# Kernel tuning notes

Measured on AMD Instinct MI355X. Metric: run time of the kernel, lower is better.

The kernel has to match this reference:

```python
import jax, jax.numpy as jnp
import numpy as np

B, N, D, H, ND = 16, 512, 768, 12, 32
DK = D // H  # 64
GRID = 11    # hard-coded 11x11 patch grid in SpatialCirclePosition.patch


def setup_inputs() -> dict:
    key = jax.random.key(0)
    ks = jax.random.split(key, 10)
    features = jax.random.normal(ks[0], (B, N, D), dtype=jnp.float32)
    boxes = jax.random.uniform(ks[1], (B, N, 4), dtype=jnp.float32)  # normalized [0,1]
    sizes_wh = jax.random.randint(ks[2], (B, 2), 512, 1024).astype(jnp.int32)
    image_sizes = jnp.concatenate([sizes_wh, sizes_wh], axis=-1)  # (B,4) = [w,h,w,h]
    s = 0.02
    Wq = jax.random.normal(ks[3], (D, D), dtype=jnp.float32) * s
    Wk = jax.random.normal(ks[4], (D, D), dtype=jnp.float32) * s
    Wv = jax.random.normal(ks[5], (D, D), dtype=jnp.float32) * s
    Wo = jax.random.normal(ks[6], (D, D), dtype=jnp.float32) * s
    bq = jnp.zeros((D,), jnp.float32); bk = jnp.zeros((D,), jnp.float32)
    bv = jnp.zeros((D,), jnp.float32); bo = jnp.zeros((D,), jnp.float32)
    gamma = jnp.ones((D,), jnp.float32); beta = jnp.zeros((D,), jnp.float32)
    dist_emb = jax.random.normal(ks[7], (ND, H), dtype=jnp.float32) * s
    return {"features": features, "boxes": boxes, "image_sizes": image_sizes,
            "Wq": Wq, "bq": bq, "Wk": Wk, "bk": bk, "Wv": Wv, "bv": bv,
            "Wo": Wo, "bo": bo, "gamma": gamma, "beta": beta, "dist_emb": dist_emb}


def _patch_bins(boxes_norm, image_sizes):
    # boxes_norm: (B,N,4) in [0,1]; image_sizes: (B,4)=[w,h,w,h] int
    sizes_f = image_sizes.astype(jnp.float32)
    boxes = boxes_norm * sizes_f[:, None, :]                       # pixel boxes
    spa = jnp.floor_divide(sizes_f[:, :2], 11.0)                   # (B,2) size_per_area
    lb = jnp.arange(GRID, dtype=jnp.float32)                       # (11,)
    hb = lb + 1.0
    wlb = lb[None, :] * spa[:, 0:1]; whb = hb[None, :] * spa[:, 0:1]   # (B,11)
    hlb = lb[None, :] * spa[:, 1:2]; hhb = hb[None, :] * spa[:, 1:2]
    cx = jnp.floor_divide(boxes[..., 0] + boxes[..., 2], 2.0)      # (B,N)
    cy = jnp.floor_divide(boxes[..., 1] + boxes[..., 3], 2.0)
    mx = (wlb[:, None, :] <= cx[..., None]) & (cx[..., None] <= whb[:, None, :])  # (B,N,11)
    my = (hlb[:, None, :] <= cy[..., None]) & (cy[..., None] <= hhb[:, None, :])
    px = jnp.argmax(mx.astype(jnp.float32), axis=-1)               # (B,N) int
    py = jnp.argmax(my.astype(jnp.float32), axis=-1)
    return px.astype(jnp.float32), py.astype(jnp.float32)


def _dist_bins(boxes_norm, image_sizes):
    px, py = _patch_bins(boxes_norm, image_sizes)
    dx = px[:, None, :] - px[:, :, None]                           # (B,N,N)
    dy = py[:, None, :] - py[:, :, None]
    dist = jnp.sqrt(dx * dx + dy * dy) * 2.0
    return dist.astype(jnp.int32)                                  # truncation == .long()


def reference(features, boxes, image_sizes, Wq, bq, Wk, bk, Wv, bv, Wo, bo, gamma, beta, dist_emb):
    # LayerNorm(d_model), eps matches torch default 1e-5
    mu = jnp.mean(features, axis=-1, keepdims=True)
    var = jnp.mean(jnp.square(features - mu), axis=-1, keepdims=True)
    x = (features - mu) * jax.lax.rsqrt(var + 1e-5) * gamma + beta

    bins = _dist_bins(boxes, image_sizes)                          # (B,N,N) int32
    dist_bias = dist_emb[bins]                                     # (B,N,N,H)
    dist_bias = jnp.transpose(dist_bias, (0, 3, 1, 2))             # (B,H,N,N)

    bsz, nq, _ = x.shape
    q = (x @ Wq.T + bq).reshape(bsz, nq, H, DK).transpose(0, 2, 1, 3)  # (B,H,N,DK)
    k = (x @ Wk.T + bk).reshape(bsz, nq, H, DK).transpose(0, 2, 1, 3)
    v = (x @ Wv.T + bv).reshape(bsz, nq, H, DK).transpose(0, 2, 1, 3)

    att = jnp.einsum('bhqd,bhkd->bhqk', q, k) / np.sqrt(DK).astype(np.float32)
    att = jax.nn.softmax(att + dist_bias, axis=-1)                 # (B,H,N,N)
    out = jnp.einsum('bhqk,bhkd->bhqd', att, v)
    out = out.transpose(0, 2, 1, 3).reshape(bsz, nq, H * DK)
    out = out @ Wo.T + bo
    return out, att
```

## Files before the change

### kernel.cpp

```cpp
#include <hip/hip_runtime.h>
#include <hip/hip_bf16.h>

typedef unsigned char uchar;
typedef __attribute__((ext_vector_type(8))) short bf16x8;
typedef __attribute__((ext_vector_type(4))) float f32x4;

__device__ __forceinline__ unsigned short f2bf(float f) {
  union { float f; unsigned int u; } v; v.f = f;
  unsigned int u = v.u + 0x7fffu + ((v.u >> 16) & 1u);
  return (unsigned short)(u >> 16);
}

__device__ __forceinline__ void async_cp16(void* lds, const void* g) {
  __builtin_amdgcn_global_load_lds(
      (const __attribute__((address_space(1))) unsigned int*)g,
      (__attribute__((address_space(3))) unsigned int*)lds, 16, 0, 0);
}

__global__ void pxpy_kernel(const float* __restrict__ boxes, const int* __restrict__ isz,
                            float* __restrict__ px, float* __restrict__ py) {
  int idx = blockIdx.x * 256 + threadIdx.x;
  int b = idx >> 9;
  float w = (float)isz[b * 4 + 0];
  float h = (float)isz[b * 4 + 1];
  float b0 = boxes[idx * 4 + 0] * w;
  float b1 = boxes[idx * 4 + 1] * h;
  float b2 = boxes[idx * 4 + 2] * w;
  float b3 = boxes[idx * 4 + 3] * h;
  float spw = floorf(w / 11.0f);
  float sph = floorf(h / 11.0f);
  float cx = floorf((b0 + b2) * 0.5f);
  float cy = floorf((b1 + b3) * 0.5f);
  int pxi = 0, pyi = 0;
  bool fx = false, fy = false;
  for (int j = 0; j < 11; ++j) {
    float jf = (float)j;
    if (!fx && jf * spw <= cx && cx <= (jf + 1.0f) * spw) { pxi = j; fx = true; }
    if (!fy && jf * sph <= cy && cy <= (jf + 1.0f) * sph) { pyi = j; fy = true; }
  }
  px[idx] = (float)pxi;
  py[idx] = (float)pyi;
}

__global__ void bins_kernel(const float* __restrict__ px, const float* __restrict__ py,
                            uchar* __restrict__ bins) {
  int r = blockIdx.x;
  int j = threadIdx.x;
  int b = r >> 9;
  float pxq = px[r], pyq = py[r];
  float dx = px[b * 512 + j] - pxq;
  float dy = py[b * 512 + j] - pyq;
  float d = sqrtf(dx * dx + dy * dy) * 2.0f;
  bins[(size_t)r * 512 + j] = (uchar)(int)d;
}

__global__ __launch_bounds__(256) void ln_kernel(const float* __restrict__ f,
                                                 const float* __restrict__ gamma,
                                                 const float* __restrict__ beta,
                                                 unsigned short* __restrict__ x) {
  const int r = blockIdx.x;
  const int t = threadIdx.x;
  const float* row = f + (size_t)r * 768;
  float e0 = row[t], e1 = row[t + 256], e2 = row[t + 512];
  float s = e0 + e1 + e2;
#pragma unroll
  for (int off = 32; off > 0; off >>= 1) s += __shfl_down(s, off);
  __shared__ float red[4];
  const int wid = t >> 6;
  if ((t & 63) == 0) red[wid] = s;
  __syncthreads();
  float mean = (red[0] + red[1] + red[2] + red[3]) * (1.0f / 768.0f);
  __syncthreads();
  float d0 = e0 - mean, d1 = e1 - mean, d2 = e2 - mean;
  float v = d0 * d0 + d1 * d1 + d2 * d2;
#pragma unroll
  for (int off = 32; off > 0; off >>= 1) v += __shfl_down(v, off);
  if ((t & 63) == 0) red[wid] = v;
  __syncthreads();
  float var = (red[0] + red[1] + red[2] + red[3]) * (1.0f / 768.0f);
  float rs = rsqrtf(var + 1e-5f);
  x[(size_t)r * 768 + t]       = f2bf(d0 * rs * gamma[t] + beta[t]);
  x[(size_t)r * 768 + t + 256] = f2bf(d1 * rs * gamma[t + 256] + beta[t + 256]);
  x[(size_t)r * 768 + t + 512] = f2bf(d2 * rs * gamma[t + 512] + beta[t + 512]);
}

__global__ void wprep_kernel(const float* __restrict__ Wq, const float* __restrict__ Wk,
                             const float* __restrict__ Wv, const float* __restrict__ Wo,
                             const float* __restrict__ bq, const float* __restrict__ bk,
                             const float* __restrict__ bv,
                             unsigned short* __restrict__ wcat, unsigned short* __restrict__ wo,
                             float* __restrict__ bcat) {
  int idx = blockIdx.x * 256 + threadIdx.x;
  if (idx < 1769472) {
    int n = idx / 768, k = idx % 768;
    float v = (n < 768) ? Wq[n * 768 + k]
            : (n < 1536) ? Wk[(n - 768) * 768 + k]
                         : Wv[(n - 1536) * 768 + k];
    wcat[idx] = f2bf(v);
  } else {
    int j = idx - 1769472;
    wo[j] = f2bf(Wo[j]);
  }
  if (idx < 2304)
    bcat[idx] = (idx < 768) ? bq[idx] : (idx < 1536) ? bk[idx - 768] : bv[idx - 1536];
}

template <bool OUTF32>
__global__ __launch_bounds__(256) void gemm_bt(const unsigned short* __restrict__ A,
                                               const unsigned short* __restrict__ Bt,
                                               const float* __restrict__ bias,
                                               void* __restrict__ Cout, int K, int ldc) {
  __shared__ unsigned short a_lds[2][128 * 32];
  __shared__ unsigned short b_lds[2][128 * 32];
  const int m0 = blockIdx.x * 128, n0 = blockIdx.y * 128;
  const int tid = threadIdx.x;
  const int lane = tid & 63, wid = tid >> 6;
  const int ln = lane & 15, quad = lane >> 4;
  const int wm = (wid & 1) * 64, wn = (wid >> 1) * 64;
  f32x4 acc[16] = {};
  const int nk = K >> 5;
#pragma unroll
  for (int rep = 0; rep < 2; ++rep) {
    int c = rep * 256 + tid;
    int row = c >> 2, e0 = (c & 3) << 3;
    async_cp16(&a_lds[0][c * 8], A + (size_t)(m0 + row) * K + e0);
    async_cp16(&b_lds[0][c * 8], Bt + (size_t)(n0 + row) * K + e0);
  }
  __syncthreads();
  for (int kc = 0; kc < nk; ++kc) {
    const int cur = kc & 1;
    if (kc + 1 < nk) {
      const int k0 = (kc + 1) << 5;
#pragma unroll
      for (int rep = 0; rep < 2; ++rep) {
        int c = rep * 256 + tid;
        int row = c >> 2, e0 = (c & 3) << 3;
        async_cp16(&a_lds[cur ^ 1][c * 8], A + (size_t)(m0 + row) * K + k0 + e0);
        async_cp16(&b_lds[cur ^ 1][c * 8], Bt + (size_t)(n0 + row) * K + k0 + e0);
      }
    }
    bf16x8 af[4], bfr[4];
#pragma unroll
    for (int i = 0; i < 4; ++i)
      af[i] = *(const bf16x8*)&a_lds[cur][(wm + i * 16 + ln) * 32 + quad * 8];
#pragma unroll
    for (int j = 0; j < 4; ++j)
      bfr[j] = *(const bf16x8*)&b_lds[cur][(wn + j * 16 + ln) * 32 + quad * 8];
#pragma unroll
    for (int i = 0; i < 4; ++i)
#pragma unroll
      for (int j = 0; j < 4; ++j)
        acc[i * 4 + j] = __builtin_amdgcn_mfma_f32_16x16x32_bf16(af[i], bfr[j], acc[i * 4 + j], 0, 0, 0);
    __syncthreads();
  }
#pragma unroll
  for (int i = 0; i < 4; ++i)
#pragma unroll
    for (int j = 0; j < 4; ++j)
#pragma unroll
      for (int r = 0; r < 4; ++r) {
        int rr = m0 + wm + i * 16 + quad * 4 + r;
        int cc = n0 + wn + j * 16 + ln;
        float v = acc[i * 4 + j][r] + bias[cc];
        if (OUTF32) ((float*)Cout)[(size_t)rr * ldc + cc] = v;
        else ((unsigned short*)Cout)[(size_t)rr * ldc + cc] = f2bf(v);
      }
}

__global__ __launch_bounds__(256) void attn_fused(const unsigned short* __restrict__ qkv,
                                                  const uchar* __restrict__ bins,
                                                  const float* __restrict__ dist_emb,
                                                  float* __restrict__ att,
                                                  unsigned short* __restrict__ attnout) {
  const int bidx = blockIdx.x;
  const int qt = bidx & 7;
  const int h = (bidx >> 3) % 12;
  const int b = bidx / 96;
  __shared__ unsigned short qs[64 * 72];
  __shared__ unsigned short ks[2][64 * 72];
  __shared__ float demb[32];
  const int tid = threadIdx.x;
  const int lane = tid & 63, wid = tid >> 6;
  const int ln = lane & 15, quad = lane >> 4;
  if (tid < 32) demb[tid] = dist_emb[tid * 12 + h];

  {
    int i0 = tid >> 3, e0 = (tid & 7) * 8;
    *(uint4*)&qs[i0 * 72 + e0] =
        *(const uint4*)(qkv + (size_t)(b * 512 + qt * 64 + i0) * 2304 + h * 64 + e0);
    *(uint4*)&qs[(i0 + 32) * 72 + e0] =
        *(const uint4*)(qkv + (size_t)(b * 512 + qt * 64 + i0 + 32) * 2304 + h * 64 + e0);
  }
  const int si = tid >> 3, se = (tid & 7) * 8;
  const unsigned short* kbase = qkv + (size_t)(b * 512) * 2304 + 768 + h * 64 + se;
  const unsigned short* vbase = qkv + (size_t)(b * 512) * 2304 + 1536 + h * 64 + se;
  uint4 kr0 = *(const uint4*)(kbase + (size_t)si * 2304);
  uint4 kr1 = *(const uint4*)(kbase + (size_t)(si + 32) * 2304);
  __syncthreads();
  bf16x8 a0 = *(const bf16x8*)&qs[(wid * 16 + ln) * 72 + quad * 8];
  bf16x8 a1 = *(const bf16x8*)&qs[(wid * 16 + ln) * 72 + 32 + quad * 8];
  *(uint4*)&ks[0][si * 72 + se] = kr0;
  *(uint4*)&ks[0][(si + 32) * 72 + se] = kr1;
  __syncthreads();
  f32x4 acc[32] = {};
  for (int kc = 0; kc < 8; ++kc) {
    const unsigned short* cur = ks[kc & 1];
    if (kc < 7) {
      kr0 = *(const uint4*)(kbase + (size_t)((kc + 1) * 64 + si) * 2304);
      kr1 = *(const uint4*)(kbase + (size_t)((kc + 1) * 64 + si + 32) * 2304);
    }
    __builtin_amdgcn_s_setprio(1);
#pragma unroll
    for (int t = 0; t < 4; ++t) {
      bf16x8 b0 = *(const bf16x8*)&cur[(t * 16 + ln) * 72 + quad * 8];
      bf16x8 b1 = *(const bf16x8*)&cur[(t * 16 + ln) * 72 + 32 + quad * 8];
      acc[kc * 4 + t] = __builtin_amdgcn_mfma_f32_16x16x32_bf16(a0, b0, acc[kc * 4 + t], 0, 0, 0);
      acc[kc * 4 + t] = __builtin_amdgcn_mfma_f32_16x16x32_bf16(a1, b1, acc[kc * 4 + t], 0, 0, 0);
    }
    __builtin_amdgcn_s_setprio(0);
    if (kc < 7) {
      unsigned short* nxt = ks[(kc + 1) & 1];
      *(uint4*)&nxt[si * 72 + se] = kr0;
      *(uint4*)&nxt[(si + 32) * 72 + se] = kr1;
      __syncthreads();
    }
  }
  uint4 vr0 = *(const uint4*)(vbase + (size_t)si * 2304);
  uint4 vr1 = *(const uint4*)(vbase + (size_t)(si + 32) * 2304);

  const int brow0 = qt * 64 + wid * 16 + quad * 4;
  const uchar* binb = bins + (size_t)b * 512 * 512;
#pragma unroll
  for (int i = 0; i < 32; ++i) {
    int col = (i >> 2) * 64 + (i & 3) * 16 + ln;
#pragma unroll
    for (int r = 0; r < 4; ++r) {
      int bin = binb[(size_t)(brow0 + r) * 512 + col];
      acc[i][r] = acc[i][r] * 0.125f + demb[bin];
    }
  }
  float inv[4];
#pragma unroll
  for (int r = 0; r < 4; ++r) {
    float m = -1e30f;
#pragma unroll
    for (int i = 0; i < 32; ++i) m = fmaxf(m, acc[i][r]);
    m = fmaxf(m, __shfl_xor(m, 1));
    m = fmaxf(m, __shfl_xor(m, 2));
    m = fmaxf(m, __shfl_xor(m, 4));
    m = fmaxf(m, __shfl_xor(m, 8));
    float s = 0.f;
#pragma unroll
    for (int i = 0; i < 32; ++i) { float p = __expf(acc[i][r] - m); acc[i][r] = p; s += p; }
    s += __shfl_xor(s, 1); s += __shfl_xor(s, 2); s += __shfl_xor(s, 4); s += __shfl_xor(s, 8);
    inv[r] = 1.0f / s;
  }
#pragma unroll
  for (int i = 0; i < 32; ++i)
#pragma unroll
    for (int r = 0; r < 4; ++r) acc[i][r] *= inv[r];

  {
    const unsigned short* xs = (const unsigned short*)&vr0;
#pragma unroll
    for (int j = 0; j < 8; ++j) {
      int d = se + j;
      ks[0][d * 72 + (si ^ (((d >> 3) & 7) << 3))] = xs[j];
    }
    xs = (const unsigned short*)&vr1;
#pragma unroll
    for (int j = 0; j < 8; ++j) {
      int d = se + j;
      ks[0][d * 72 + ((si + 32) ^ (((d >> 3) & 7) << 3))] = xs[j];
    }
  }
  __syncthreads();
  f32x4 acc_o[4] = {};
  float* ob = att + (size_t)((b * 12 + h) * 512) * 512;
  for (int kc = 0; kc < 8; ++kc) {
    const unsigned short* cur = ks[kc & 1];
    if (kc < 7) {
      vr0 = *(const uint4*)(vbase + (size_t)((kc + 1) * 64 + si) * 2304);
      vr1 = *(const uint4*)(vbase + (size_t)((kc + 1) * 64 + si + 32) * 2304);
    }
#pragma unroll
    for (int t = 0; t < 4; ++t)
#pragma unroll
      for (int r = 0; r < 4; ++r) {
        int row = wid * 16 + quad * 4 + r;
        int col = (t * 16 + ln) ^ (((row >> 2) & 7) << 3);
        qs[row * 72 + col] = f2bf(acc[kc * 4 + t][r]);
      }
    __builtin_amdgcn_s_setprio(1);
#pragma unroll
    for (int kk = 0; kk < 2; ++kk) {
      int prow = wid * 16 + ln;
      int pcol = (kk * 32 + quad * 8) ^ (((prow >> 2) & 7) << 3);
      bf16x8 af = *(const bf16x8*)&qs[prow * 72 + pcol];
#pragma unroll
      for (int ct = 0; ct < 4; ++ct) {
        int d = ct * 16 + ln;
        int vcol = (kk * 32 + quad * 8) ^ (((d >> 3) & 7) << 3);
        bf16x8 bg = *(const bf16x8*)&cur[d * 72 + vcol];
        acc_o[ct] = __builtin_amdgcn_mfma_f32_16x16x32_bf16(af, bg, acc_o[ct], 0, 0, 0);
      }
    }
    __builtin_amdgcn_s_setprio(0);
#pragma unroll
    for (int t = 0; t < 4; ++t)
#pragma unroll
      for (int r = 0; r < 4; ++r)
        ob[(size_t)(brow0 + r) * 512 + kc * 64 + t * 16 + ln] = acc[kc * 4 + t][r];
    if (kc < 7) {
      unsigned short* nxt = ks[(kc + 1) & 1];
      const unsigned short* xs = (const unsigned short*)&vr0;
#pragma unroll
      for (int j = 0; j < 8; ++j) {
        int d = se + j;
        nxt[d * 72 + (si ^ (((d >> 3) & 7) << 3))] = xs[j];
      }
      xs = (const unsigned short*)&vr1;
#pragma unroll
      for (int j = 0; j < 8; ++j) {
        int d = se + j;
        nxt[d * 72 + ((si + 32) ^ (((d >> 3) & 7) << 3))] = xs[j];
      }
      __syncthreads();
    }
  }
#pragma unroll
  for (int ct = 0; ct < 4; ++ct)
#pragma unroll
    for (int r = 0; r < 4; ++r) {
      int m = b * 512 + qt * 64 + wid * 16 + quad * 4 + r;
      int cc = h * 64 + ct * 16 + ln;
      attnout[(size_t)m * 768 + cc] = f2bf(acc_o[ct][r]);
    }
}

extern "C" void kernel_launch(void* const* d_in, const int* in_sizes, int n_in,
                              void* d_out, int out_size, void* d_ws, size_t ws_size,
                              hipStream_t stream) {
  const float* features = (const float*)d_in[0];
  const float* boxes    = (const float*)d_in[1];
  const int*   isz      = (const int*)d_in[2];
  const float* Wq = (const float*)d_in[3];
  const float* bq = (const float*)d_in[4];
  const float* Wk = (const float*)d_in[5];
  const float* bk = (const float*)d_in[6];
  const float* Wv = (const float*)d_in[7];
  const float* bv = (const float*)d_in[8];
  const float* Wo = (const float*)d_in[9];
  const float* bo = (const float*)d_in[10];
  const float* gamma = (const float*)d_in[11];
  const float* beta  = (const float*)d_in[12];
  const float* dist_emb = (const float*)d_in[13];

  float* out = (float*)d_out;
  float* att = out + (size_t)8192 * 768;

  char* w = (char*)d_ws;
  float* px = (float*)w;          w += 8192 * 4;
  float* py = (float*)w;          w += 8192 * 4;
  uchar* bins = (uchar*)w;        w += (size_t)16 * 512 * 512;
  unsigned short* x = (unsigned short*)w;       w += (size_t)8192 * 768 * 2;
  unsigned short* wcat = (unsigned short*)w;    w += (size_t)2304 * 768 * 2;
  unsigned short* wo = (unsigned short*)w;      w += (size_t)768 * 768 * 2;
  float* bcat = (float*)w;                      w += 2304 * 4;
  unsigned short* qkv = (unsigned short*)w;     w += (size_t)8192 * 2304 * 2;
  unsigned short* attnout = (unsigned short*)w; w += (size_t)8192 * 768 * 2;

  pxpy_kernel<<<32, 256, 0, stream>>>(boxes, isz, px, py);
  bins_kernel<<<8192, 512, 0, stream>>>(px, py, bins);
  ln_kernel<<<8192, 256, 0, stream>>>(features, gamma, beta, x);
  wprep_kernel<<<9216, 256, 0, stream>>>(Wq, Wk, Wv, Wo, bq, bk, bv, wcat, wo, bcat);
  gemm_bt<false><<<dim3(64, 18), 256, 0, stream>>>(x, wcat, bcat, qkv, 768, 2304);
  attn_fused<<<1536, 256, 0, stream>>>(qkv, bins, dist_emb, att, attnout);
  gemm_bt<true><<<dim3(64, 6), 256, 0, stream>>>(attnout, wo, bo, out, 768, 768);
}
```

Measured before the change: 431.2 us.

## Fuse distance-bin computation into attention via packed patch coords and LDS LUT

Removes the bins_kernel and its 4 MB uint8 bins tensor. Each patch's (px,py) is packed into a ushort, and the attention kernel builds a 21x21 per-head lookup table of dist_emb values indexed by (dx,dy) in LDS. The bias is then gathered from that table with a per-row offset instead of being read from global bins. This cuts one kernel launch and the bins write and read traffic, at the cost of a small table build in every attention block and extra LDS reads.

Result: faster. 397.7 us (-7.8%).

```diff
diff --git a/kernel.cpp b/kernel.cpp
--- a/kernel.cpp
+++ b/kernel.cpp
@@ -18,7 +18,7 @@
 }
 
 __global__ void pxpy_kernel(const float* __restrict__ boxes, const int* __restrict__ isz,
-                            float* __restrict__ px, float* __restrict__ py) {
+                            unsigned short* __restrict__ ppk) {
   int idx = blockIdx.x * 256 + threadIdx.x;
   int b = idx >> 9;
   float w = (float)isz[b * 4 + 0];
@@ -38,20 +38,7 @@
     if (!fx && jf * spw <= cx && cx <= (jf + 1.0f) * spw) { pxi = j; fx = true; }
     if (!fy && jf * sph <= cy && cy <= (jf + 1.0f) * sph) { pyi = j; fy = true; }
   }
-  px[idx] = (float)pxi;
-  py[idx] = (float)pyi;
-}
-
-__global__ void bins_kernel(const float* __restrict__ px, const float* __restrict__ py,
-                            uchar* __restrict__ bins) {
-  int r = blockIdx.x;
-  int j = threadIdx.x;
-  int b = r >> 9;
-  float pxq = px[r], pyq = py[r];
-  float dx = px[b * 512 + j] - pxq;
-  float dy = py[b * 512 + j] - pyq;
-  float d = sqrtf(dx * dx + dy * dy) * 2.0f;
-  bins[(size_t)r * 512 + j] = (uchar)(int)d;
+  ppk[idx] = (unsigned short)(pxi | (pyi << 8));
 }
 
 __global__ __launch_bounds__(256) void ln_kernel(const float* __restrict__ f,
@@ -168,7 +155,7 @@
 }
 
 __global__ __launch_bounds__(256) void attn_fused(const unsigned short* __restrict__ qkv,
-                                                  const uchar* __restrict__ bins,
+                                                  const unsigned short* __restrict__ ppk,
                                                   const float* __restrict__ dist_emb,
                                                   float* __restrict__ att,
                                                   unsigned short* __restrict__ attnout) {
@@ -178,11 +165,18 @@
   const int b = bidx / 96;
   __shared__ unsigned short qs[64 * 72];
   __shared__ unsigned short ks[2][64 * 72];
-  __shared__ float demb[32];
+  __shared__ float lut[448];
+  __shared__ unsigned short pklds[512];
   const int tid = threadIdx.x;
   const int lane = tid & 63, wid = tid >> 6;
   const int ln = lane & 15, quad = lane >> 4;
-  if (tid < 32) demb[tid] = dist_emb[tid * 12 + h];
+  for (int t = tid; t < 441; t += 256) {
+    int dx = t / 21 - 10, dy = t % 21 - 10;
+    int bin = (int)(sqrtf((float)(dx * dx + dy * dy)) * 2.0f);
+    lut[t] = dist_emb[bin * 12 + h];
+  }
+  if (tid < 64)
+    *(uint4*)&pklds[tid * 8] = *(const uint4*)(ppk + (size_t)b * 512 + tid * 8);
 
   {
     int i0 = tid >> 3, e0 = (tid & 7) * 8;
@@ -229,14 +223,20 @@
   uint4 vr1 = *(const uint4*)(vbase + (size_t)(si + 32) * 2304);
 
   const int brow0 = qt * 64 + wid * 16 + quad * 4;
-  const uchar* binb = bins + (size_t)b * 512 * 512;
+  int cr[4];
+#pragma unroll
+  for (int r = 0; r < 4; ++r) {
+    int pq = pklds[brow0 + r];
+    cr[r] = 220 - (pq & 255) * 21 - (pq >> 8);
+  }
 #pragma unroll
   for (int i = 0; i < 32; ++i) {
     int col = (i >> 2) * 64 + (i & 3) * 16 + ln;
+    int pk = pklds[col];
+    int base = (pk & 255) * 21 + (pk >> 8);
 #pragma unroll
     for (int r = 0; r < 4; ++r) {
-      int bin = binb[(size_t)(brow0 + r) * 512 + col];
-      acc[i][r] = acc[i][r] * 0.125f + demb[bin];
+      acc[i][r] = acc[i][r] * 0.125f + lut[base + cr[r]];
     }
   }
   float inv[4];
@@ -360,9 +360,7 @@
   float* att = out + (size_t)8192 * 768;
 
   char* w = (char*)d_ws;
-  float* px = (float*)w;          w += 8192 * 4;
-  float* py = (float*)w;          w += 8192 * 4;
-  uchar* bins = (uchar*)w;        w += (size_t)16 * 512 * 512;
+  unsigned short* ppk = (unsigned short*)w;     w += 8192 * 2;
   unsigned short* x = (unsigned short*)w;       w += (size_t)8192 * 768 * 2;
   unsigned short* wcat = (unsigned short*)w;    w += (size_t)2304 * 768 * 2;
   unsigned short* wo = (unsigned short*)w;      w += (size_t)768 * 768 * 2;
@@ -370,11 +368,10 @@
   unsigned short* qkv = (unsigned short*)w;     w += (size_t)8192 * 2304 * 2;
   unsigned short* attnout = (unsigned short*)w; w += (size_t)8192 * 768 * 2;
 
-  pxpy_kernel<<<32, 256, 0, stream>>>(boxes, isz, px, py);
-  bins_kernel<<<8192, 512, 0, stream>>>(px, py, bins);
+  pxpy_kernel<<<32, 256, 0, stream>>>(boxes, isz, ppk);
   ln_kernel<<<8192, 256, 0, stream>>>(features, gamma, beta, x);
   wprep_kernel<<<9216, 256, 0, stream>>>(Wq, Wk, Wv, Wo, bq, bk, bv, wcat, wo, bcat);
   gemm_bt<false><<<dim3(64, 18), 256, 0, stream>>>(x, wcat, bcat, qkv, 768, 2304);
-  attn_fused<<<1536, 256, 0, stream>>>(qkv, bins, dist_emb, att, attnout);
+  attn_fused<<<1536, 256, 0, stream>>>(qkv, ppk, dist_emb, att, attnout);
   gemm_bt<true><<<dim3(64, 6), 256, 0, stream>>>(attnout, wo, bo, out, 768, 768);
 }
```
